# Optimization experiments

Measured on AMD Instinct MI355X. Metric: run time of the kernel, lower is better.

## Reference

```python
import math
import jax, jax.numpy as jnp
import numpy as np

IN_DIM = 1024
OUT_DIM = 1024
K = 32
N_BANDS = 3
TOTAL_K = K * N_BANDS
LAYER_IDX = 0
NUM_LAYERS = 1
SCALE = math.sqrt(2.0 / (IN_DIM + OUT_DIM))


def _make_pos():
    l_val = (LAYER_IDX + 1) / (NUM_LAYERS + 1)
    i_idx = (jnp.arange(IN_DIM, dtype=jnp.float32) + 1) / (IN_DIM + 1)
    j_idx = (jnp.arange(OUT_DIM, dtype=jnp.float32) + 1) / (OUT_DIM + 1)
    ii, jj = jnp.meshgrid(i_idx, j_idx, indexing='ij')
    pos = jnp.stack([ii, jj, jnp.full_like(ii, l_val)], axis=-1)
    return pos.reshape(-1, 3)  # (in_dim*out_dim, 3)


def setup_inputs() -> dict:
    key = jax.random.key(0)
    kx, ko, kp, ka = jax.random.split(key, 4)
    x = jax.random.normal(kx, (4096, IN_DIM), dtype=jnp.float32)
    # omega with per-band scaling (1 + band*3), matching the torch init
    band_scales = jnp.repeat(1.0 + 3.0 * jnp.arange(N_BANDS, dtype=jnp.float32), K)
    omega = jax.random.normal(ko, (TOTAL_K, 3), dtype=jnp.float32) * band_scales[:, None]
    phi = jax.random.normal(kp, (TOTAL_K,), dtype=jnp.float32) * math.pi
    alpha = jax.random.normal(ka, (2 * TOTAL_K,), dtype=jnp.float32) * 0.01 / (1.0 + jnp.arange(2 * TOTAL_K, dtype=jnp.float32))
    bias = jnp.zeros((OUT_DIM,), dtype=jnp.float32)
    pos = _make_pos()
    return {"x": x, "omega": omega, "phi": phi, "alpha": alpha, "bias": bias, "pos": pos}


def reference(x, omega, phi, alpha, bias, pos):
    # args: (in*out, total_k)
    args = pos @ omega.T + phi
    # features @ alpha == sin(args)@alpha[:K2//2] + cos(args)@alpha[K2//2:]
    a_sin, a_cos = alpha[:TOTAL_K], alpha[TOTAL_K:]
    w_flat = jnp.sin(args) @ a_sin + jnp.cos(args) @ a_cos  # (in*out,)
    # torch: w = flat.reshape(in, out).T * scale; F.linear(x, w) = x @ w.T
    w_t = w_flat.reshape(IN_DIM, OUT_DIM) * SCALE  # == w.T
    return x @ w_t + bias
```

## Files before the change

kernel.cpp:

```cpp
#include <hip/hip_runtime.h>
#include <hip/hip_bf16.h>


#define IN_DIM   1024
#define OUT_DIM  1024
#define NBANDS   96
#define KTAB     192
#define MX       4096
#define SCALE_W  0.03125f

typedef __bf16 bf16x8 __attribute__((ext_vector_type(8)));
typedef float  f32x4  __attribute__((ext_vector_type(4)));

#define AS1 __attribute__((address_space(1)))
#define AS3 __attribute__((address_space(3)))

__device__ __forceinline__ void gload_lds16(const void* g, void* l) {
  __builtin_amdgcn_global_load_lds((AS1 void*)(g), (AS3 void*)(l), 16, 0, 0);
}

__global__ void convert_x(const float* __restrict__ x,
                          __hip_bfloat16* __restrict__ xb) {
  int i = (blockIdx.x * 256 + threadIdx.x) * 4;
  float4 v = *(const float4*)(x + i);
  ushort4 o;
  __hip_bfloat16 t;
  t = __float2bfloat16(v.x); o.x = *(unsigned short*)&t;
  t = __float2bfloat16(v.y); o.y = *(unsigned short*)&t;
  t = __float2bfloat16(v.z); o.z = *(unsigned short*)&t;
  t = __float2bfloat16(v.w); o.w = *(unsigned short*)&t;
  *(ushort4*)(xb + i) = o;
}

__global__ void build_tables(const float* __restrict__ omega,
                             const float* __restrict__ phi,
                             const float* __restrict__ alpha,
                             const float* __restrict__ pos,
                             __hip_bfloat16* __restrict__ Ta,
                             __hip_bfloat16* __restrict__ Tb) {
  int idx = blockIdx.x * 256 + threadIdx.x;
  int half = IN_DIM * NBANDS;
  bool isB = idx >= half;
  int r = isB ? (idx - half) : idx;
  int i = r / NBANDS;
  int t = r - i * NBANDS;
  float lv = pos[2];
  if (!isB) {
    float iv = pos[(size_t)i * OUT_DIM * 3];
    float u = omega[3 * t] * iv + omega[3 * t + 2] * lv + phi[t];
    float su, cu;
    sincosf(u, &su, &cu);
    float as = alpha[t], ac = alpha[NBANDS + t];
    float P = SCALE_W * (as * su + ac * cu);
    float Q = SCALE_W * (as * cu - ac * su);
    Ta[(size_t)i * KTAB + 2 * t]     = __float2bfloat16(P);
    Ta[(size_t)i * KTAB + 2 * t + 1] = __float2bfloat16(Q);
  } else {
    float jv = pos[3 * i + 1];
    float v = omega[3 * t + 1] * jv;
    float sv, cv;
    sincosf(v, &sv, &cv);
    Tb[(size_t)i * KTAB + 2 * t]     = __float2bfloat16(cv);
    Tb[(size_t)i * KTAB + 2 * t + 1] = __float2bfloat16(sv);
  }
}

template <int OUT_BF16>
__global__ __launch_bounds__(256)
void gemm_bt(const __hip_bfloat16* __restrict__ A,
             const __hip_bfloat16* __restrict__ B,
             void* __restrict__ Cout,
             const float* __restrict__ bias,
             int M, int N, int K) {
  __shared__ __align__(16) __hip_bfloat16 As[128 * 32];
  __shared__ __align__(16) __hip_bfloat16 Bs[128 * 32];
  const int tid  = threadIdx.x;
  const int lane = tid & 63;
  const int wave = tid >> 6;
  const int wr = wave >> 1, wc = wave & 1;
  const int m0 = blockIdx.y * 128;
  const int n0 = blockIdx.x * 128;

  f32x4 acc[4][4] = {};

  const int lr = lane & 15;
  const int lk = (lane >> 4) * 8;

  for (int k0 = 0; k0 < K; k0 += 32) {
#pragma unroll
    for (int q = 0; q < 2; ++q) {
      int f = q * 256 + tid;
      int r = f >> 2;
      int c16 = f & 3;
      gload_lds16(A + (size_t)(m0 + r) * K + k0 + c16 * 8,
                  (char*)As + (size_t)f * 16);
      gload_lds16(B + (size_t)(n0 + r) * K + k0 + c16 * 8,
                  (char*)Bs + (size_t)f * 16);
    }
    __syncthreads();

    bf16x8 af[4], bfr[4];
#pragma unroll
    for (int mi = 0; mi < 4; ++mi)
      af[mi] = *(const bf16x8*)&As[(wr * 64 + mi * 16 + lr) * 32 + lk];
#pragma unroll
    for (int ni = 0; ni < 4; ++ni)
      bfr[ni] = *(const bf16x8*)&Bs[(wc * 64 + ni * 16 + lr) * 32 + lk];
#pragma unroll
    for (int mi = 0; mi < 4; ++mi)
#pragma unroll
      for (int ni = 0; ni < 4; ++ni)
        acc[mi][ni] = __builtin_amdgcn_mfma_f32_16x16x32_bf16(
            af[mi], bfr[ni], acc[mi][ni], 0, 0, 0);
    __syncthreads();
  }

#pragma unroll
  for (int mi = 0; mi < 4; ++mi) {
#pragma unroll
    for (int ni = 0; ni < 4; ++ni) {
#pragma unroll
      for (int r = 0; r < 4; ++r) {
        int row = m0 + wr * 64 + mi * 16 + (lane >> 4) * 4 + r;
        int col = n0 + wc * 64 + ni * 16 + lr;
        float v = acc[mi][ni][r];
        if (OUT_BF16) {
          ((__hip_bfloat16*)Cout)[(size_t)row * N + col] = __float2bfloat16(v);
        } else {
          ((float*)Cout)[(size_t)row * N + col] = v + bias[col];
        }
      }
    }
  }
}

extern "C" void kernel_launch(void* const* d_in, const int* in_sizes, int n_in,
                              void* d_out, int out_size, void* d_ws, size_t ws_size,
                              hipStream_t stream) {
  const float* x     = (const float*)d_in[0];
  const float* omega = (const float*)d_in[1];
  const float* phi   = (const float*)d_in[2];
  const float* alpha = (const float*)d_in[3];
  const float* bias  = (const float*)d_in[4];
  const float* pos   = (const float*)d_in[5];
  float* out = (float*)d_out;
  (void)in_sizes; (void)n_in; (void)out_size; (void)ws_size;

  char* ws = (char*)d_ws;
  __hip_bfloat16* Xb = (__hip_bfloat16*)(ws);
  __hip_bfloat16* WT = (__hip_bfloat16*)(ws + 8388608);
  __hip_bfloat16* Ta = (__hip_bfloat16*)(ws + 10485760);
  __hip_bfloat16* Tb = (__hip_bfloat16*)(ws + 10878976);

  convert_x<<<dim3((MX * IN_DIM) / (256 * 4)), dim3(256), 0, stream>>>(x, Xb);
  build_tables<<<dim3((2 * IN_DIM * NBANDS) / 256), dim3(256), 0, stream>>>(
      omega, phi, alpha, pos, Ta, Tb);
  gemm_bt<1><<<dim3(OUT_DIM / 128, IN_DIM / 128), dim3(256), 0, stream>>>(
      Tb, Ta, (void*)WT, nullptr, IN_DIM, OUT_DIM, KTAB);
  gemm_bt<0><<<dim3(OUT_DIM / 128, MX / 128), dim3(256), 0, stream>>>(
      Xb, WT, (void*)out, bias, MX, OUT_DIM, IN_DIM);
}
```

Baseline: 116.6 us.

## Reassociate low-rank weight product to multiply x by factor tables first

The dense 1024x1024 weight is no longer materialized. The kernel now computes Y = X·TaTᵀ (4096x192) with split-K partials, reduces them to bf16, then computes Y·Tbᵀ plus bias. This removes most of the GEMM FLOPs, because the weight has rank 192. It also folds the fp32→bf16 conversion of x into the first GEMM's load path and computes pos coordinates analytically instead of reading the pos input. In exchange it adds split-K partial-sum traffic, an extra reduce kernel, and a second bf16 rounding of the intermediate Y.

```diff
diff --git a/kernel.cpp b/kernel.cpp
--- a/kernel.cpp
+++ b/kernel.cpp
@@ -1,5 +1,6 @@
 #include <hip/hip_runtime.h>
 #include <hip/hip_bf16.h>
+#include <math.h>
 
 
 #define IN_DIM   1024
@@ -8,6 +9,7 @@
 #define KTAB     192
 #define MX       4096
 #define SCALE_W  0.03125f
+#define NSPLIT   4
 
 typedef __bf16 bf16x8 __attribute__((ext_vector_type(8)));
 typedef float  f32x4  __attribute__((ext_vector_type(4)));
@@ -19,95 +21,166 @@
   __builtin_amdgcn_global_load_lds((AS1 void*)(g), (AS3 void*)(l), 16, 0, 0);
 }
 
-__global__ void convert_x(const float* __restrict__ x,
-                          __hip_bfloat16* __restrict__ xb) {
-  int i = (blockIdx.x * 256 + threadIdx.x) * 4;
-  float4 v = *(const float4*)(x + i);
-  ushort4 o;
-  __hip_bfloat16 t;
-  t = __float2bfloat16(v.x); o.x = *(unsigned short*)&t;
-  t = __float2bfloat16(v.y); o.y = *(unsigned short*)&t;
-  t = __float2bfloat16(v.z); o.z = *(unsigned short*)&t;
-  t = __float2bfloat16(v.w); o.w = *(unsigned short*)&t;
-  *(ushort4*)(xb + i) = o;
+__device__ __forceinline__ unsigned short bf16bits(float f) {
+  __hip_bfloat16 b = __float2bfloat16(f);
+  return *(unsigned short*)&b;
 }
 
 __global__ void build_tables(const float* __restrict__ omega,
                              const float* __restrict__ phi,
                              const float* __restrict__ alpha,
-                             const float* __restrict__ pos,
-                             __hip_bfloat16* __restrict__ Ta,
+                             __hip_bfloat16* __restrict__ TaT,
                              __hip_bfloat16* __restrict__ Tb) {
-  int idx = blockIdx.x * 256 + threadIdx.x;
-  int half = IN_DIM * NBANDS;
-  bool isB = idx >= half;
-  int r = isB ? (idx - half) : idx;
-  int i = r / NBANDS;
-  int t = r - i * NBANDS;
-  float lv = pos[2];
-  if (!isB) {
-    float iv = pos[(size_t)i * OUT_DIM * 3];
-    float u = omega[3 * t] * iv + omega[3 * t + 2] * lv + phi[t];
+  const int t = blockIdx.x;
+  const float ox = omega[3 * t], oy = omega[3 * t + 1], oz = omega[3 * t + 2];
+  const float uc = oz * 0.5f + phi[t];
+  const float as_ = alpha[t], ac = alpha[NBANDS + t];
+#pragma unroll
+  for (int s = 0; s < 4; ++s) {
+    const int i = s * 256 + threadIdx.x;
+    const float coord = (float)(i + 1) / 1025.0f;
     float su, cu;
-    sincosf(u, &su, &cu);
-    float as = alpha[t], ac = alpha[NBANDS + t];
-    float P = SCALE_W * (as * su + ac * cu);
-    float Q = SCALE_W * (as * cu - ac * su);
-    Ta[(size_t)i * KTAB + 2 * t]     = __float2bfloat16(P);
-    Ta[(size_t)i * KTAB + 2 * t + 1] = __float2bfloat16(Q);
-  } else {
-    float jv = pos[3 * i + 1];
-    float v = omega[3 * t + 1] * jv;
+    sincosf(ox * coord + uc, &su, &cu);
+    const float P = SCALE_W * (as_ * su + ac * cu);
+    const float Q = SCALE_W * (as_ * cu - ac * su);
+    TaT[(size_t)(2 * t) * IN_DIM + i]     = __float2bfloat16(P);
+    TaT[(size_t)(2 * t + 1) * IN_DIM + i] = __float2bfloat16(Q);
     float sv, cv;
-    sincosf(v, &sv, &cv);
+    sincosf(oy * coord, &sv, &cv);
     Tb[(size_t)i * KTAB + 2 * t]     = __float2bfloat16(cv);
     Tb[(size_t)i * KTAB + 2 * t + 1] = __float2bfloat16(sv);
   }
 }
 
-template <int OUT_BF16>
+__global__ __launch_bounds__(512)
+void gemm_xta(const float* __restrict__ X,
+              const __hip_bfloat16* __restrict__ TaT,
+              float* __restrict__ Pp) {
+  __shared__ __align__(16) __hip_bfloat16 As[64 * 32];
+  __shared__ __align__(16) __hip_bfloat16 Bs[192 * 32];
+  const int tid  = threadIdx.x;
+  const int lane = tid & 63;
+  const int wave = tid >> 6;
+  const int wr = wave >> 2;
+  const int wc = wave & 3;
+  const int m0  = blockIdx.y * 64;
+  const int ks0 = blockIdx.z * (IN_DIM / NSPLIT);
+
+  f32x4 acc[2][3] = {};
+  const int lr = lane & 15;
+  const int lk = (lane >> 4) * 8;
+
+  for (int k0 = 0; k0 < IN_DIM / NSPLIT; k0 += 32) {
+    {
+      const int r = tid >> 3;
+      const int c4 = tid & 7;
+      float4 v = *(const float4*)(X + (size_t)(m0 + r) * IN_DIM + ks0 + k0 + c4 * 4);
+      ushort4 o;
+      o.x = bf16bits(v.x); o.y = bf16bits(v.y);
+      o.z = bf16bits(v.z); o.w = bf16bits(v.w);
+      *(ushort4*)((char*)As + (size_t)r * 64 + c4 * 8) = o;
+    }
+    {
+      const int r = tid >> 2, c16 = tid & 3;
+      gload_lds16(TaT + (size_t)r * IN_DIM + ks0 + k0 + c16 * 8,
+                  (char*)Bs + (size_t)tid * 16);
+      if (tid < 256) {
+        const int c2 = 512 + tid;
+        const int r2 = c2 >> 2, c162 = c2 & 3;
+        gload_lds16(TaT + (size_t)r2 * IN_DIM + ks0 + k0 + c162 * 8,
+                    (char*)Bs + (size_t)c2 * 16);
+      }
+    }
+    __syncthreads();
+
+    bf16x8 af[2], bfr[3];
+#pragma unroll
+    for (int mi = 0; mi < 2; ++mi)
+      af[mi] = *(const bf16x8*)&As[(wr * 32 + mi * 16 + lr) * 32 + lk];
+#pragma unroll
+    for (int ni = 0; ni < 3; ++ni)
+      bfr[ni] = *(const bf16x8*)&Bs[(wc * 48 + ni * 16 + lr) * 32 + lk];
+#pragma unroll
+    for (int mi = 0; mi < 2; ++mi)
+#pragma unroll
+      for (int ni = 0; ni < 3; ++ni)
+        acc[mi][ni] = __builtin_amdgcn_mfma_f32_16x16x32_bf16(
+            af[mi], bfr[ni], acc[mi][ni], 0, 0, 0);
+    __syncthreads();
+  }
+
+  float* P = Pp + (size_t)blockIdx.z * (MX * KTAB);
+#pragma unroll
+  for (int mi = 0; mi < 2; ++mi)
+#pragma unroll
+    for (int ni = 0; ni < 3; ++ni)
+#pragma unroll
+      for (int r = 0; r < 4; ++r) {
+        const int row = m0 + wr * 32 + mi * 16 + (lane >> 4) * 4 + r;
+        const int col = wc * 48 + ni * 16 + lr;
+        P[(size_t)row * KTAB + col] = acc[mi][ni][r];
+      }
+}
+
+__global__ void reduce_y(const float* __restrict__ Pp,
+                         __hip_bfloat16* __restrict__ Y) {
+  const int i = (blockIdx.x * 256 + threadIdx.x) * 4;
+  const int S = MX * KTAB;
+  float4 a = *(const float4*)(Pp + i);
+  float4 b = *(const float4*)(Pp + S + i);
+  float4 c = *(const float4*)(Pp + 2 * S + i);
+  float4 d = *(const float4*)(Pp + 3 * S + i);
+  ushort4 o;
+  o.x = bf16bits(a.x + b.x + c.x + d.x);
+  o.y = bf16bits(a.y + b.y + c.y + d.y);
+  o.z = bf16bits(a.z + b.z + c.z + d.z);
+  o.w = bf16bits(a.w + b.w + c.w + d.w);
+  *(ushort4*)(Y + i) = o;
+}
+
 __global__ __launch_bounds__(256)
-void gemm_bt(const __hip_bfloat16* __restrict__ A,
-             const __hip_bfloat16* __restrict__ B,
-             void* __restrict__ Cout,
-             const float* __restrict__ bias,
-             int M, int N, int K) {
-  __shared__ __align__(16) __hip_bfloat16 As[128 * 32];
+void gemm_out(const __hip_bfloat16* __restrict__ Y,
+              const __hip_bfloat16* __restrict__ Tb,
+              float* __restrict__ out,
+              const float* __restrict__ bias) {
+  __shared__ __align__(16) __hip_bfloat16 As[64 * 32];
   __shared__ __align__(16) __hip_bfloat16 Bs[128 * 32];
   const int tid  = threadIdx.x;
   const int lane = tid & 63;
   const int wave = tid >> 6;
-  const int wr = wave >> 1, wc = wave & 1;
-  const int m0 = blockIdx.y * 128;
+  const int wr = wave >> 1;
+  const int wc = wave & 1;
+  const int m0 = blockIdx.y * 64;
   const int n0 = blockIdx.x * 128;
 
-  f32x4 acc[4][4] = {};
-
+  f32x4 acc[2][4] = {};
   const int lr = lane & 15;
   const int lk = (lane >> 4) * 8;
 
-  for (int k0 = 0; k0 < K; k0 += 32) {
+  for (int k0 = 0; k0 < KTAB; k0 += 32) {
+    {
+      const int r = tid >> 2, c16 = tid & 3;
+      gload_lds16(Y + (size_t)(m0 + r) * KTAB + k0 + c16 * 8,
+                  (char*)As + (size_t)tid * 16);
+    }
 #pragma unroll
     for (int q = 0; q < 2; ++q) {
-      int f = q * 256 + tid;
-      int r = f >> 2;
-      int c16 = f & 3;
-      gload_lds16(A + (size_t)(m0 + r) * K + k0 + c16 * 8,
-                  (char*)As + (size_t)f * 16);
-      gload_lds16(B + (size_t)(n0 + r) * K + k0 + c16 * 8,
+      const int f = q * 256 + tid;
+      const int r = f >> 2, c16 = f & 3;
+      gload_lds16(Tb + (size_t)(n0 + r) * KTAB + k0 + c16 * 8,
                   (char*)Bs + (size_t)f * 16);
     }
     __syncthreads();
 
-    bf16x8 af[4], bfr[4];
-#pragma unroll
-    for (int mi = 0; mi < 4; ++mi)
-      af[mi] = *(const bf16x8*)&As[(wr * 64 + mi * 16 + lr) * 32 + lk];
+    bf16x8 af[2], bfr[4];
+#pragma unroll
+    for (int mi = 0; mi < 2; ++mi)
+      af[mi] = *(const bf16x8*)&As[(wr * 32 + mi * 16 + lr) * 32 + lk];
 #pragma unroll
     for (int ni = 0; ni < 4; ++ni)
       bfr[ni] = *(const bf16x8*)&Bs[(wc * 64 + ni * 16 + lr) * 32 + lk];
 #pragma unroll
-    for (int mi = 0; mi < 4; ++mi)
+    for (int mi = 0; mi < 2; ++mi)
 #pragma unroll
       for (int ni = 0; ni < 4; ++ni)
         acc[mi][ni] = __builtin_amdgcn_mfma_f32_16x16x32_bf16(
@@ -116,22 +189,15 @@
   }
 
 #pragma unroll
-  for (int mi = 0; mi < 4; ++mi) {
-#pragma unroll
-    for (int ni = 0; ni < 4; ++ni) {
+  for (int mi = 0; mi < 2; ++mi)
+#pragma unroll
+    for (int ni = 0; ni < 4; ++ni)
 #pragma unroll
       for (int r = 0; r < 4; ++r) {
-        int row = m0 + wr * 64 + mi * 16 + (lane >> 4) * 4 + r;
-        int col = n0 + wc * 64 + ni * 16 + lr;
-        float v = acc[mi][ni][r];
-        if (OUT_BF16) {
-          ((__hip_bfloat16*)Cout)[(size_t)row * N + col] = __float2bfloat16(v);
-        } else {
-          ((float*)Cout)[(size_t)row * N + col] = v + bias[col];
-        }
+        const int row = m0 + wr * 32 + mi * 16 + (lane >> 4) * 4 + r;
+        const int col = n0 + wc * 64 + ni * 16 + lr;
+        out[(size_t)row * OUT_DIM + col] = acc[mi][ni][r] + bias[col];
       }
-    }
-  }
 }
 
 extern "C" void kernel_launch(void* const* d_in, const int* in_sizes, int n_in,
@@ -142,21 +208,17 @@
   const float* phi   = (const float*)d_in[2];
   const float* alpha = (const float*)d_in[3];
   const float* bias  = (const float*)d_in[4];
-  const float* pos   = (const float*)d_in[5];
   float* out = (float*)d_out;
   (void)in_sizes; (void)n_in; (void)out_size; (void)ws_size;
 
   char* ws = (char*)d_ws;
-  __hip_bfloat16* Xb = (__hip_bfloat16*)(ws);
-  __hip_bfloat16* WT = (__hip_bfloat16*)(ws + 8388608);
-  __hip_bfloat16* Ta = (__hip_bfloat16*)(ws + 10485760);
-  __hip_bfloat16* Tb = (__hip_bfloat16*)(ws + 10878976);
-
-  convert_x<<<dim3((MX * IN_DIM) / (256 * 4)), dim3(256), 0, stream>>>(x, Xb);
-  build_tables<<<dim3((2 * IN_DIM * NBANDS) / 256), dim3(256), 0, stream>>>(
-      omega, phi, alpha, pos, Ta, Tb);
-  gemm_bt<1><<<dim3(OUT_DIM / 128, IN_DIM / 128), dim3(256), 0, stream>>>(
-      Tb, Ta, (void*)WT, nullptr, IN_DIM, OUT_DIM, KTAB);
-  gemm_bt<0><<<dim3(OUT_DIM / 128, MX / 128), dim3(256), 0, stream>>>(
-      Xb, WT, (void*)out, bias, MX, OUT_DIM, IN_DIM);
-}
+  float* Pp           = (float*)(ws);
+  __hip_bfloat16* Y   = (__hip_bfloat16*)(ws + 12582912);
+  __hip_bfloat16* TaT = (__hip_bfloat16*)(ws + 14155776);
+  __hip_bfloat16* Tb  = (__hip_bfloat16*)(ws + 14548992);
+
+  build_tables<<<dim3(NBANDS), dim3(256), 0, stream>>>(omega, phi, alpha, TaT, Tb);
+  gemm_xta<<<dim3(1, MX / 64, NSPLIT), dim3(512), 0, stream>>>(x, TaT, Pp);
+  reduce_y<<<dim3((MX * KTAB) / (256 * 4)), dim3(256), 0, stream>>>(Pp, Y);
+  gemm_out<<<dim3(OUT_DIM / 128, MX / 64), dim3(256), 0, stream>>>(Y, Tb, out, bias);
+}
```

After: 102.4 us. 12.2% less time.
